# Optimization experiments

Hardware: AMD Instinct MI355X
Metric: run time of the kernel (lower is better)

## Reference

```python
import jax, jax.numpy as jnp
import numpy as np

STRIDE = 2

def setup_inputs() -> dict:
    key = jax.random.key(0)
    k1, k2 = jax.random.split(key)
    x = jax.random.normal(k1, (4, 64, 16, 16, 16), dtype=jnp.float32)
    weight = jax.random.normal(k2, (32, 64, 3, 3, 3), dtype=jnp.float32)
    return {"x": x, "weight": weight}


def reference(x, weight):
    # Faithful to ConvTranspose3dMPS.forward:
    # 1) nearest-neighbor upsample by `stride` via repeat
    # 2) per (out,in) channel pair: circular conv via FFT, summed over in
    B, C, D, H, W = x.shape
    s = STRIDE
    Co, Ci, k, _, _ = weight.shape
    Du, Hu, Wu = D * s, H * s, W * s

    # view->repeat->view == repeat each voxel s times along each spatial axis
    xu = jnp.repeat(jnp.repeat(jnp.repeat(x, s, axis=2), s, axis=3), s, axis=4)

    # FFT of upsampled input (computed once, not per channel pair)
    fx = jnp.fft.fftn(xu, axes=(2, 3, 4))  # [B, Ci, Du, Hu, Wu] complex

    # torch.fft.fftn(weight[i,j], s=x.shape[-3:]) zero-pads kernel at the end
    wpad = jnp.zeros((Co, Ci, Du, Hu, Wu), dtype=weight.dtype)
    wpad = wpad.at[:, :, :k, :k, :k].set(weight)
    fw = jnp.fft.fftn(wpad, axes=(2, 3, 4))  # [Co, Ci, Du, Hu, Wu] complex

    # sum over input channels in frequency domain, take real part of ifft
    fo = jnp.einsum('bjdhw,ijdhw->bidhw', fx, fw)
    out = jnp.fft.ifftn(fo, axes=(2, 3, 4)).real.astype(x.dtype)
    return out
```

## Files before the change

kernel.cpp:

```cpp
#include <hip/hip_runtime.h>


typedef float f32x16 __attribute__((ext_vector_type(16)));
typedef short s16x8 __attribute__((ext_vector_type(8)));

#define CI  64
#define CO  32
#define QV  4096
#define XT_ELEMS (4 * QV * CI)
#define WE_ELEMS (4 * 16 * 8 * 32 * 8)
#define WE_PP    (16 * 8 * 32 * 8)

__device__ __forceinline__ unsigned short f32_to_bf16_rne(float f) {
    union { float f; unsigned u; } v; v.f = f;
    unsigned u = v.u;
    unsigned r = u + 0x7FFFu + ((u >> 16) & 1u);
    return (unsigned short)(r >> 16);
}

__global__ __launch_bounds__(256)
void prep_kernel(const float* __restrict__ x, const float* __restrict__ weight,
                 unsigned short* __restrict__ xT, unsigned short* __restrict__ WeG) {
    const int blk = blockIdx.x;
    {
        const int tid = blk * 256 + threadIdx.x;
        const int b  = tid >> 15;
        const int rem = tid & 32767;
        const int c  = rem >> 12;
        const int q  = rem & 4095;
        const float* xb = x + b * (CI * QV) + q;
        s16x8 pk;
        #pragma unroll
        for (int e = 0; e < 8; ++e)
            pk[e] = (short)f32_to_bf16_rne(xb[(c * 8 + e) * QV]);
        *reinterpret_cast<s16x8*>(xT + (((size_t)(b * 8 + c)) * QV + q) * 8) = pk;
    }
    if (threadIdx.x < 32) {
        const int tid = blk * 32 + threadIdx.x;
        const int p = tid >> 11, i = (tid >> 6) & 31, j = tid & 63;
        const int pd = p >> 2, ph = (p >> 1) & 1, pw = p & 1;
        const int pp = pd * 2 + ph;

        const float* wp = weight + (i * CI + j) * 27;
        float wv[27];
        #pragma unroll
        for (int k = 0; k < 27; ++k) wv[k] = wp[k];

        float t1[2][9];
        #pragma unroll
        for (int m = 0; m < 9; ++m) {
            t1[0][m] = pd ? (wv[m] + wv[9 + m]) : wv[m];
            t1[1][m] = pd ? wv[18 + m] : (wv[9 + m] + wv[18 + m]);
        }
        float t2[2][2][3];
        #pragma unroll
        for (int td = 0; td < 2; ++td)
            #pragma unroll
            for (int m = 0; m < 3; ++m) {
                t2[td][0][m] = ph ? (t1[td][m] + t1[td][3 + m]) : t1[td][m];
                t2[td][1][m] = ph ? (t1[td][6 + m]) : (t1[td][3 + m] + t1[td][6 + m]);
            }

        const int c = j >> 3, e = j & 7;
        #pragma unroll
        for (int td = 0; td < 2; ++td)
            #pragma unroll
            for (int th = 0; th < 2; ++th) {
                float a0 = pw ? (t2[td][th][0] + t2[td][th][1]) : t2[td][th][0];
                float a1 = pw ? t2[td][th][2] : (t2[td][th][1] + t2[td][th][2]);
                const int tA = td * 4 + th * 2;
                const int plane0 = pw * 8 + tA;
                WeG[(((pp * 16 + plane0) * 8 + c) * 32 + i) * 8 + e]     = f32_to_bf16_rne(a0);
                WeG[(((pp * 16 + plane0 + 1) * 8 + c) * 32 + i) * 8 + e] = f32_to_bf16_rne(a1);
            }
    }
}

__global__ __launch_bounds__(256)
void convt3d_mfma_kernel(const unsigned short* __restrict__ xT,
                         const unsigned short* __restrict__ WeG,
                         float* __restrict__ out) {
    __shared__ unsigned short we_lds[WE_PP];

    const int blk = blockIdx.x;
    const int pp  = blk >> 7;
    const int T   = blk & 127;
    const int pd = pp >> 1, ph = pp & 1;

    {
        const char* src = (const char*)(WeG + pp * WE_PP);
        char* dst = (char*)we_lds;
        #pragma unroll
        for (int pass = 0; pass < 16; ++pass) {
            const int off = pass * 4096 + threadIdx.x * 16;
            *reinterpret_cast<s16x8*>(dst + off) =
                *reinterpret_cast<const s16x8*>(src + off);
        }
    }
    __syncthreads();

    const int b    = threadIdx.x >> 6;
    const int l    = threadIdx.x & 63;
    const int n    = l & 31;
    const int half = l >> 5;

    const int qd = T >> 3;
    const int qh = (T & 7) * 2 + (n >> 4);
    const int qw = n & 15;

    f32x16 acc0 = {};
    f32x16 acc1 = {};
    const unsigned short* xTb = xT + (size_t)b * (CI * QV);

    #pragma unroll
    for (int t = 0; t < 8; ++t) {
        const int td = t >> 2, th = (t >> 1) & 1, tw = t & 1;
        const int dd = (qd - td) & 15, hh = (qh - th) & 15, ww = (qw - tw) & 15;
        const int qpos = (dd * 16 + hh) * 16 + ww;
        #pragma unroll
        for (int ks = 0; ks < 4; ++ks) {
            const int c = 2 * ks + half;
            const s16x8 bfrag = *reinterpret_cast<const s16x8*>(
                xTb + ((size_t)c * QV + qpos) * 8);
            const s16x8 a0 = *reinterpret_cast<const s16x8*>(
                we_lds + ((t * 8 + c) * 32 + n) * 8);
            const s16x8 a1 = *reinterpret_cast<const s16x8*>(
                we_lds + (((8 + t) * 8 + c) * 32 + n) * 8);
            acc0 = __builtin_amdgcn_mfma_f32_32x32x16_bf16(a0, bfrag, acc0, 0, 0, 0);
            acc1 = __builtin_amdgcn_mfma_f32_32x32x16_bf16(a1, bfrag, acc1, 0, 0, 0);
        }
    }

    const int d = 2 * qd + pd, h = 2 * qh + ph, wq = 2 * qw;
    #pragma unroll
    for (int r = 0; r < 16; ++r) {
        const int m = (r & 3) + 8 * (r >> 2) + 4 * half;
        float2 v; v.x = acc0[r]; v.y = acc1[r];
        *reinterpret_cast<float2*>(out + (((size_t)b * CO + m) * 32 + d) * 1024 + h * 32 + wq) = v;
    }
}

extern "C" void kernel_launch(void* const* d_in, const int* in_sizes, int n_in,
                              void* d_out, int out_size, void* d_ws, size_t ws_size,
                              hipStream_t stream) {
    const float* x      = (const float*)d_in[0];
    const float* weight = (const float*)d_in[1];
    float* out          = (float*)d_out;

    unsigned short* xT = (unsigned short*)d_ws;
    unsigned short* We = xT + XT_ELEMS;

    prep_kernel<<<512, 256, 0, stream>>>(x, weight, xT, We);
    convt3d_mfma_kernel<<<512, 256, 0, stream>>>(xT, We, out);
}
```

Measured before the change: 18.17 us.

## Stage input halo tile in LDS via direct global-to-LDS loads, double output tile per block

The conv kernel now loads a halo tile of the transposed input (5 rows × 2 depth planes per batch-channel group) into LDS alongside the weights, using global_load_lds direct copies, instead of reading B-fragments straight from global memory. Each block covers twice as many output rows with four accumulators reusing the same A fragments, and the grid is halved to 256 blocks. This raises weight and input reuse and cuts redundant global reads. In exchange it uses about 144KB of LDS per block, which limits occupancy to one block per CU, and leaves fewer blocks to fill the machine.

```diff
diff --git a/kernel.cpp b/kernel.cpp
--- a/kernel.cpp
+++ b/kernel.cpp
@@ -8,14 +8,22 @@
 #define CO  32
 #define QV  4096
 #define XT_ELEMS (4 * QV * CI)
-#define WE_ELEMS (4 * 16 * 8 * 32 * 8)
 #define WE_PP    (16 * 8 * 32 * 8)
+#define WE_BYTES 65536
+#define X_BYTES  81920
+#define LDS_BYTES (WE_BYTES + X_BYTES)
 
 __device__ __forceinline__ unsigned short f32_to_bf16_rne(float f) {
     union { float f; unsigned u; } v; v.f = f;
     unsigned u = v.u;
     unsigned r = u + 0x7FFFu + ((u >> 16) & 1u);
     return (unsigned short)(r >> 16);
+}
+
+__device__ __forceinline__ void gload_lds16(const void* g, void* l) {
+    __builtin_amdgcn_global_load_lds(
+        (__attribute__((address_space(1))) unsigned int*)g,
+        (__attribute__((address_space(3))) unsigned int*)l, 16, 0, 0);
 }
 
 __global__ __launch_bounds__(256)
@@ -80,63 +88,93 @@
 void convt3d_mfma_kernel(const unsigned short* __restrict__ xT,
                          const unsigned short* __restrict__ WeG,
                          float* __restrict__ out) {
-    __shared__ unsigned short we_lds[WE_PP];
+    __shared__ __align__(16) char smem[LDS_BYTES];
+    unsigned short* we_lds = (unsigned short*)smem;
+    char* x_lds = smem + WE_BYTES;
 
     const int blk = blockIdx.x;
-    const int pp  = blk >> 7;
-    const int T   = blk & 127;
+    const int pp  = blk >> 6;
+    const int T2  = blk & 63;
     const int pd = pp >> 1, ph = pp & 1;
+    const int qd = T2 >> 2, qhq = T2 & 3;
+
+    const int w    = threadIdx.x >> 6;
+    const int lane = threadIdx.x & 63;
 
     {
         const char* src = (const char*)(WeG + pp * WE_PP);
-        char* dst = (char*)we_lds;
         #pragma unroll
-        for (int pass = 0; pass < 16; ++pass) {
-            const int off = pass * 4096 + threadIdx.x * 16;
-            *reinterpret_cast<s16x8*>(dst + off) =
-                *reinterpret_cast<const s16x8*>(src + off);
+        for (int k = 0; k < 16; ++k) {
+            const int off = (w * 16 + k) * 1024 + lane * 16;
+            gload_lds16(src + off, smem + off);
         }
     }
+    {
+        const char* srcb = (const char*)xT;
+        #pragma unroll
+        for (int k = 0; k < 20; ++k) {
+            const int chunk = w * 20 + k;
+            const int seg   = chunk * 4 + (lane >> 4);
+            const int bc    = seg / 10;
+            const int dhh   = seg - bc * 10;
+            const int dd_i  = (dhh >= 5) ? 1 : 0;
+            const int hh_i  = dhh - dd_i * 5;
+            const int dd = (qd - 1 + dd_i) & 15;
+            const int hh = (qhq * 4 - 1 + hh_i) & 15;
+            const long srcoff = ((long)bc * QV + (dd * 16 + hh) * 16 + (lane & 15)) * 16;
+            gload_lds16(srcb + srcoff, x_lds + chunk * 1024 + lane * 16);
+        }
+    }
+    asm volatile("s_waitcnt vmcnt(0)" ::: "memory");
     __syncthreads();
 
-    const int b    = threadIdx.x >> 6;
-    const int l    = threadIdx.x & 63;
-    const int n    = l & 31;
-    const int half = l >> 5;
+    const int b    = w;
+    const int n    = lane & 31;
+    const int half = lane >> 5;
+    const int qw   = n & 15;
+    const int hsel = n >> 4;
 
-    const int qd = T >> 3;
-    const int qh = (T & 7) * 2 + (n >> 4);
-    const int qw = n & 15;
-
-    f32x16 acc0 = {};
-    f32x16 acc1 = {};
-    const unsigned short* xTb = xT + (size_t)b * (CI * QV);
+    f32x16 acc00 = {}, acc01 = {};
+    f32x16 acc10 = {}, acc11 = {};
 
     #pragma unroll
     for (int t = 0; t < 8; ++t) {
         const int td = t >> 2, th = (t >> 1) & 1, tw = t & 1;
-        const int dd = (qd - td) & 15, hh = (qh - th) & 15, ww = (qw - tw) & 15;
-        const int qpos = (dd * 16 + hh) * 16 + ww;
+        const int dd_i = 1 - td;
+        const int ww = (qw - tw) & 15;
+        const int hbase = dd_i * 5 + hsel + 1 - th;
         #pragma unroll
         for (int ks = 0; ks < 4; ++ks) {
-            const int c = 2 * ks + half;
-            const s16x8 bfrag = *reinterpret_cast<const s16x8*>(
-                xTb + ((size_t)c * QV + qpos) * 8);
+            const int c  = 2 * ks + half;
+            const int bc = b * 8 + c;
+            const s16x8 b0 = *reinterpret_cast<const s16x8*>(
+                x_lds + (bc * 10 + hbase) * 256 + ww * 16);
+            const s16x8 b1 = *reinterpret_cast<const s16x8*>(
+                x_lds + (bc * 10 + hbase + 2) * 256 + ww * 16);
             const s16x8 a0 = *reinterpret_cast<const s16x8*>(
                 we_lds + ((t * 8 + c) * 32 + n) * 8);
             const s16x8 a1 = *reinterpret_cast<const s16x8*>(
                 we_lds + (((8 + t) * 8 + c) * 32 + n) * 8);
-            acc0 = __builtin_amdgcn_mfma_f32_32x32x16_bf16(a0, bfrag, acc0, 0, 0, 0);
-            acc1 = __builtin_amdgcn_mfma_f32_32x32x16_bf16(a1, bfrag, acc1, 0, 0, 0);
+            acc00 = __builtin_amdgcn_mfma_f32_32x32x16_bf16(a0, b0, acc00, 0, 0, 0);
+            acc01 = __builtin_amdgcn_mfma_f32_32x32x16_bf16(a1, b0, acc01, 0, 0, 0);
+            acc10 = __builtin_amdgcn_mfma_f32_32x32x16_bf16(a0, b1, acc10, 0, 0, 0);
+            acc11 = __builtin_amdgcn_mfma_f32_32x32x16_bf16(a1, b1, acc11, 0, 0, 0);
         }
     }
 
-    const int d = 2 * qd + pd, h = 2 * qh + ph, wq = 2 * qw;
+    const int d = 2 * qd + pd;
     #pragma unroll
-    for (int r = 0; r < 16; ++r) {
-        const int m = (r & 3) + 8 * (r >> 2) + 4 * half;
-        float2 v; v.x = acc0[r]; v.y = acc1[r];
-        *reinterpret_cast<float2*>(out + (((size_t)b * CO + m) * 32 + d) * 1024 + h * 32 + wq) = v;
+    for (int tau = 0; tau < 2; ++tau) {
+        const int h = 2 * (4 * qhq + 2 * tau + hsel) + ph;
+        float* ob = out + ((size_t)b * CO) * 32768 + d * 1024 + h * 32 + 2 * qw;
+        #pragma unroll
+        for (int r = 0; r < 16; ++r) {
+            const int m = (r & 3) + 8 * (r >> 2) + 4 * half;
+            float2 v;
+            if (tau == 0) { v.x = acc00[r]; v.y = acc01[r]; }
+            else          { v.x = acc10[r]; v.y = acc11[r]; }
+            *reinterpret_cast<float2*>(ob + (size_t)m * 32768) = v;
+        }
     }
 }
 
@@ -151,5 +189,5 @@
     unsigned short* We = xT + XT_ELEMS;
 
     prep_kernel<<<512, 256, 0, stream>>>(x, weight, xT, We);
-    convt3d_mfma_kernel<<<512, 256, 0, stream>>>(xT, We, out);
+    convt3d_mfma_kernel<<<256, 256, 0, stream>>>(xT, We, out);
 }
```

Result: slower. 18.54 us (+2.0%).

## Split output-width parity across waves and load weights via global_load_lds

Applied to the files above, without the earlier changes.

Doubles the block to 512 threads so that each wave computes a single output-width parity with one accumulator instead of two. This halves per-wave MFMA work and registers while doubling wave-level parallelism. The LDS weight staging now uses direct global-to-LDS loads followed by an explicit vmcnt wait. In exchange, output stores become scalar instead of float2, and each B fragment from global memory is now loaded by two waves instead of one.

```diff
diff --git a/kernel.cpp b/kernel.cpp
--- a/kernel.cpp
+++ b/kernel.cpp
@@ -16,6 +16,12 @@
     unsigned u = v.u;
     unsigned r = u + 0x7FFFu + ((u >> 16) & 1u);
     return (unsigned short)(r >> 16);
+}
+
+__device__ __forceinline__ void gload_lds16(const void* g, void* l) {
+    __builtin_amdgcn_global_load_lds(
+        (__attribute__((address_space(1))) unsigned int*)g,
+        (__attribute__((address_space(3))) unsigned int*)l, 16, 0, 0);
 }
 
 __global__ __launch_bounds__(256)
@@ -76,11 +82,11 @@
     }
 }
 
-__global__ __launch_bounds__(256)
+__global__ __launch_bounds__(512, 4)
 void convt3d_mfma_kernel(const unsigned short* __restrict__ xT,
                          const unsigned short* __restrict__ WeG,
                          float* __restrict__ out) {
-    __shared__ unsigned short we_lds[WE_PP];
+    __shared__ __align__(16) unsigned short we_lds[WE_PP];
 
     const int blk = blockIdx.x;
     const int pp  = blk >> 7;
@@ -91,15 +97,17 @@
         const char* src = (const char*)(WeG + pp * WE_PP);
         char* dst = (char*)we_lds;
         #pragma unroll
-        for (int pass = 0; pass < 16; ++pass) {
-            const int off = pass * 4096 + threadIdx.x * 16;
-            *reinterpret_cast<s16x8*>(dst + off) =
-                *reinterpret_cast<const s16x8*>(src + off);
+        for (int pass = 0; pass < 8; ++pass) {
+            const int off = pass * 8192 + threadIdx.x * 16;
+            gload_lds16(src + off, dst + off);
         }
     }
+    asm volatile("s_waitcnt vmcnt(0)" ::: "memory");
     __syncthreads();
 
-    const int b    = threadIdx.x >> 6;
+    const int w    = threadIdx.x >> 6;
+    const int b    = w & 3;
+    const int pw   = w >> 2;
     const int l    = threadIdx.x & 63;
     const int n    = l & 31;
     const int half = l >> 5;
@@ -108,8 +116,7 @@
     const int qh = (T & 7) * 2 + (n >> 4);
     const int qw = n & 15;
 
-    f32x16 acc0 = {};
-    f32x16 acc1 = {};
+    f32x16 acc = {};
     const unsigned short* xTb = xT + (size_t)b * (CI * QV);
 
     #pragma unroll
@@ -122,21 +129,18 @@
             const int c = 2 * ks + half;
             const s16x8 bfrag = *reinterpret_cast<const s16x8*>(
                 xTb + ((size_t)c * QV + qpos) * 8);
-            const s16x8 a0 = *reinterpret_cast<const s16x8*>(
-                we_lds + ((t * 8 + c) * 32 + n) * 8);
-            const s16x8 a1 = *reinterpret_cast<const s16x8*>(
-                we_lds + (((8 + t) * 8 + c) * 32 + n) * 8);
-            acc0 = __builtin_amdgcn_mfma_f32_32x32x16_bf16(a0, bfrag, acc0, 0, 0, 0);
-            acc1 = __builtin_amdgcn_mfma_f32_32x32x16_bf16(a1, bfrag, acc1, 0, 0, 0);
+            const s16x8 a = *reinterpret_cast<const s16x8*>(
+                we_lds + (((pw * 8 + t) * 8 + c) * 32 + n) * 8);
+            acc = __builtin_amdgcn_mfma_f32_32x32x16_bf16(a, bfrag, acc, 0, 0, 0);
         }
     }
 
-    const int d = 2 * qd + pd, h = 2 * qh + ph, wq = 2 * qw;
+    const int d = 2 * qd + pd, h = 2 * qh + ph, wq = 2 * qw + pw;
+    float* ob = out + ((size_t)b * CO) * 32768 + d * 1024 + h * 32 + wq;
     #pragma unroll
     for (int r = 0; r < 16; ++r) {
         const int m = (r & 3) + 8 * (r >> 2) + 4 * half;
-        float2 v; v.x = acc0[r]; v.y = acc1[r];
-        *reinterpret_cast<float2*>(out + (((size_t)b * CO + m) * 32 + d) * 1024 + h * 32 + wq) = v;
+        ob[(size_t)m * 32768] = acc[r];
     }
 }
 
@@ -151,5 +155,5 @@
     unsigned short* We = xT + XT_ELEMS;
 
     prep_kernel<<<512, 256, 0, stream>>>(x, weight, xT, We);
-    convt3d_mfma_kernel<<<512, 256, 0, stream>>>(xT, We, out);
+    convt3d_mfma_kernel<<<512, 512, 0, stream>>>(xT, We, out);
 }
```

Measured after the change: 19.78 us. 8.9% more time.

## Load weights via direct global-to-LDS, prefetch input fragments, double threads per block

Applied to the files above, without the earlier changes.

The conv kernel now runs 512-thread blocks that cover two output tiles per weight-slice load, which halves how often the 64KB weight slice is staged into LDS. The staging uses global_load_lds, so data goes straight from global memory to LDS without passing through registers. The input fragments for the first two taps are issued before the barrier, so their latency overlaps the weight copy. In exchange the kernel has fewer blocks and each thread holds more registers for the prefetched fragments.

```diff
diff --git a/kernel.cpp b/kernel.cpp
--- a/kernel.cpp
+++ b/kernel.cpp
@@ -16,6 +16,12 @@
     unsigned u = v.u;
     unsigned r = u + 0x7FFFu + ((u >> 16) & 1u);
     return (unsigned short)(r >> 16);
+}
+
+__device__ __forceinline__ void gload_lds16(const void* g, void* l) {
+    __builtin_amdgcn_global_load_lds(
+        (__attribute__((address_space(1))) unsigned int*)g,
+        (__attribute__((address_space(3))) unsigned int*)l, 16, 0, 0);
 }
 
 __global__ __launch_bounds__(256)
@@ -76,30 +82,31 @@
     }
 }
 
-__global__ __launch_bounds__(256)
+__global__ __launch_bounds__(512)
 void convt3d_mfma_kernel(const unsigned short* __restrict__ xT,
                          const unsigned short* __restrict__ WeG,
                          float* __restrict__ out) {
-    __shared__ unsigned short we_lds[WE_PP];
+    __shared__ __align__(16) unsigned short we_lds[WE_PP];
 
     const int blk = blockIdx.x;
-    const int pp  = blk >> 7;
-    const int T   = blk & 127;
+    const int pp  = blk >> 6;
+    const int Tp  = blk & 63;
     const int pd = pp >> 1, ph = pp & 1;
 
     {
         const char* src = (const char*)(WeG + pp * WE_PP);
         char* dst = (char*)we_lds;
         #pragma unroll
-        for (int pass = 0; pass < 16; ++pass) {
-            const int off = pass * 4096 + threadIdx.x * 16;
-            *reinterpret_cast<s16x8*>(dst + off) =
-                *reinterpret_cast<const s16x8*>(src + off);
+        for (int pass = 0; pass < 8; ++pass) {
+            const int off = pass * 8192 + threadIdx.x * 16;
+            gload_lds16(src + off, dst + off);
         }
     }
-    __syncthreads();
 
-    const int b    = threadIdx.x >> 6;
+    const int w    = threadIdx.x >> 6;
+    const int b    = w & 3;
+    const int tsel = w >> 2;
+    const int T    = Tp * 2 + tsel;
     const int l    = threadIdx.x & 63;
     const int n    = l & 31;
     const int half = l >> 5;
@@ -108,9 +115,27 @@
     const int qh = (T & 7) * 2 + (n >> 4);
     const int qw = n & 15;
 
+    const unsigned short* xTb = xT + (size_t)b * (CI * QV);
+
+    s16x8 bpre[8];
+    #pragma unroll
+    for (int t = 0; t < 2; ++t) {
+        const int th = (t >> 1) & 1, tw = t & 1;
+        const int dd = qd, hh = (qh - th) & 15, ww = (qw - tw) & 15;
+        const int qpos = (dd * 16 + hh) * 16 + ww;
+        #pragma unroll
+        for (int ks = 0; ks < 4; ++ks) {
+            const int c = 2 * ks + half;
+            bpre[t * 4 + ks] = *reinterpret_cast<const s16x8*>(
+                xTb + ((size_t)c * QV + qpos) * 8);
+        }
+    }
+
+    asm volatile("s_waitcnt vmcnt(0)" ::: "memory");
+    __syncthreads();
+
     f32x16 acc0 = {};
     f32x16 acc1 = {};
-    const unsigned short* xTb = xT + (size_t)b * (CI * QV);
 
     #pragma unroll
     for (int t = 0; t < 8; ++t) {
@@ -120,8 +145,13 @@
         #pragma unroll
         for (int ks = 0; ks < 4; ++ks) {
             const int c = 2 * ks + half;
-            const s16x8 bfrag = *reinterpret_cast<const s16x8*>(
-                xTb + ((size_t)c * QV + qpos) * 8);
+            s16x8 bfrag;
+            if (t < 2) {
+                bfrag = bpre[t * 4 + ks];
+            } else {
+                bfrag = *reinterpret_cast<const s16x8*>(
+                    xTb + ((size_t)c * QV + qpos) * 8);
+            }
             const s16x8 a0 = *reinterpret_cast<const s16x8*>(
                 we_lds + ((t * 8 + c) * 32 + n) * 8);
             const s16x8 a1 = *reinterpret_cast<const s16x8*>(
@@ -151,5 +181,5 @@
     unsigned short* We = xT + XT_ELEMS;
 
     prep_kernel<<<512, 256, 0, stream>>>(x, weight, xT, We);
-    convt3d_mfma_kernel<<<512, 256, 0, stream>>>(xT, We, out);
+    convt3d_mfma_kernel<<<256, 512, 0, stream>>>(xT, We, out);
 }
```

After: 18.47 us. No clear change (+1.6%).
